# Performance work log

Hardware: AMD Instinct MI355X
Metric: run time of the kernel (lower is better)

The kernel has to match this reference:

```python
import jax, jax.numpy as jnp
import numpy as np

# module hyperparameters (init_kwargs)
WEIGHT = 2e-9
SIGMA_RGB = 0.15   # images in [0,1]; equals canonical 15/255
SIGMA_XY = 100.0
SCALE = 0.5

N, C, K, H, W = 4, 3, 21, 128, 128


def _nearest(x, oh, ow):
    """torch F.interpolate(mode='nearest'): src = floor(dst * in/out)."""
    h, w = x.shape[-2], x.shape[-1]
    iy = jnp.floor(jnp.arange(oh) * (h / oh)).astype(jnp.int32)
    ix = jnp.floor(jnp.arange(ow) * (w / ow)).astype(jnp.int32)
    return x[..., iy[:, None], ix[None, :]]


def _bilinear(x, oh, ow):
    """torch F.interpolate(mode='bilinear', align_corners=False)."""
    h, w = x.shape[-2], x.shape[-1]

    def coords(o, s):
        c = (jnp.arange(o, dtype=jnp.float32) + 0.5) * (s / o) - 0.5
        c = jnp.clip(c, 0.0, s - 1.0)
        c0 = jnp.floor(c).astype(jnp.int32)
        c1 = jnp.minimum(c0 + 1, s - 1)
        return c0, c1, c - c0

    y0, y1, wy = coords(oh, h)
    x0, x1, wx = coords(ow, w)
    wy = wy[:, None]
    wx = wx[None, :]
    v00 = x[..., y0[:, None], x0[None, :]]
    v01 = x[..., y0[:, None], x1[None, :]]
    v10 = x[..., y1[:, None], x0[None, :]]
    v11 = x[..., y1[:, None], x1[None, :]]
    top = v00 * (1.0 - wx) + v01 * wx
    bot = v10 * (1.0 - wx) + v11 * wx
    return top * (1.0 - wy) + bot * wy


def setup_inputs() -> dict:
    key = jax.random.key(0)
    k1, k2 = jax.random.split(key)
    images = jax.random.uniform(k1, (N, C, H, W), jnp.float32)
    segmentations = jax.random.uniform(k2, (N, K, H, W), jnp.float32)
    ROIs = jnp.ones((N, H, W), jnp.float32)
    return {"images": images, "segmentations": segmentations, "ROIs": ROIs}


def reference(images, segmentations, ROIs):
    oh, ow = int(H * SCALE), int(W * SCALE)
    img_s = _nearest(images, oh, ow)           # [N,3,oh,ow]
    seg_s = _bilinear(segmentations, oh, ow)   # [N,K,oh,ow]
    roi_s = _nearest(ROIs, oh, ow)             # [N,oh,ow]
    seg_m = seg_s * roi_s[:, None]             # seg * ROI (per class)
    sxy = SIGMA_XY * SCALE

    # exact dense Gaussian bilateral kernel that the permutohedral lattice
    # (bilateralfilter_batch) approximates: k(i,j) = exp(-|p_i-p_j|^2/(2 sxy^2)
    #                                                  -|I_i-I_j|^2/(2 srgb^2))
    yy, xx = jnp.meshgrid(jnp.arange(oh, dtype=jnp.float32),
                          jnp.arange(ow, dtype=jnp.float32), indexing="ij")
    pos = jnp.stack([xx, yy], 0) / sxy         # [2,oh,ow]

    def per_image(img, seg):
        feat = jnp.concatenate([pos, img / SIGMA_RGB], 0).reshape(5, -1).T  # [P,5]
        sq = jnp.sum(feat * feat, axis=-1)                                  # [P]
        d2 = jnp.maximum(sq[:, None] + sq[None, :] - 2.0 * (feat @ feat.T), 0.0)
        Wk = jnp.exp(-0.5 * d2)                                             # [P,P]
        s = seg.reshape(K, -1)                                              # [K,P]
        AS = s @ Wk                                                         # filtered seg
        return jnp.sum(s * AS)

    vals = jax.vmap(per_image)(img_s, seg_m)   # [N]
    loss = -(jnp.sum(vals)) / N                # densecrf_loss
    return WEIGHT * loss
```

## Files before the change

### kernel.cpp

```cpp
#include <hip/hip_runtime.h>

#define NIMG 4
#define CCH  3
#define KCH  21
#define HIN  128
#define WIN  128
#define OH   64
#define OW   64
#define PPX  (OH*OW)
#define NPIX (NIMG*PPX)

#define PRE2 1.20112241f

#define SEGW  24
#define FEATW 8

#define BLOCK  256
#define JCHUNK 256
#define IBLK   64

#define NSLOT  64

typedef _Float16 half_t;
typedef half_t half8  __attribute__((ext_vector_type(8)));
typedef float  f32x4v __attribute__((ext_vector_type(4)));

#define FEATH_OFF ((size_t)NPIX*SEGW*2)
#define SQF_OFF   (FEATH_OFF + (size_t)NPIX*FEATW*2)
#define SLOT_OFF  (SQF_OFF + (size_t)NPIX*4)

__global__ __launch_bounds__(BLOCK) void crf_prep(const float* __restrict__ img,
                                                  const float* __restrict__ seg,
                                                  const float* __restrict__ roi,
                                                  half_t* __restrict__ segH,
                                                  half_t* __restrict__ featH,
                                                  float* __restrict__ sqF,
                                                  float* __restrict__ slots) {
    int g  = blockIdx.x * BLOCK + threadIdx.x;
    int q  = g >> 14;
    int pl = g & (NPIX - 1);
    int n  = pl >> 12;
    int p  = pl & (PPX - 1);
    int y = p >> 6, x = p & 63;
    int y2 = 2 * y, x2 = 2 * x;

    if (q < SEGW) {
        float v = 0.0f;
        if (q < KCH) {
            const float* s0 = seg + (((size_t)n * KCH + q) * HIN + y2) * WIN + x2;
            float r = roi[((size_t)n * HIN + y2) * WIN + x2];
            v = 0.25f * (s0[0] + s0[1] + s0[WIN] + s0[WIN + 1]) * r;
        }
        segH[(size_t)pl * SEGW + q] = (half_t)v;
    } else if (q == 24) {
        float fx = (float)x * (PRE2 / 50.0f);
        float fy = (float)y * (PRE2 / 50.0f);
        const size_t ib = (((size_t)n * CCH) * HIN + y2) * WIN + x2;
        float fr = img[ib]                         * (PRE2 / 0.15f);
        float fg = img[ib + (size_t)HIN * WIN]     * (PRE2 / 0.15f);
        float fb = img[ib + 2 * (size_t)HIN * WIN] * (PRE2 / 0.15f);
        half_t h0 = (half_t)fx, h1 = (half_t)fy, h2 = (half_t)fr,
               h3 = (half_t)fg, h4 = (half_t)fb;
        half8 fh = {h0, h1, h2, h3, h4, (half_t)0, (half_t)0, (half_t)0};
        *(half8*)(featH + (size_t)pl * FEATW) = fh;
        float a0 = (float)h0, a1 = (float)h1, a2 = (float)h2,
              a3 = (float)h3, a4 = (float)h4;
        sqF[pl] = 0.5f * (a0 * a0 + a1 * a1 + a2 * a2 + a3 * a3 + a4 * a4);
    } else if (q == 25) {
        if (pl < NSLOT) slots[pl * 16] = 0.0f;
    }
}

__global__ __launch_bounds__(BLOCK, 8) void crf_main(const half_t* __restrict__ segH,
                                                     const half_t* __restrict__ featH,
                                                     const float* __restrict__ sqF,
                                                     float* __restrict__ slots) {
    const int bx = blockIdx.x;
    const int n  = blockIdx.y;

    int g = 0;
#pragma unroll
    for (int t = 1; t < 16; ++t) {
        int off = 64 * t - 2 * t * (t - 1);
        if (bx >= off) g = t;
    }
    int rem = bx - (64 * g - 2 * g * (g - 1));
    int c   = 16 - g;
    int iq  = (rem >= c) + (rem >= 2 * c) + (rem >= 3 * c);
    int I   = 4 * g + iq;
    int J   = g + (rem - iq * c);
    const bool diag = (J == (I >> 2));

    const half_t* segN  = segH  + (size_t)n * PPX * SEGW;
    const half_t* featN = featH + (size_t)n * PPX * FEATW;
    const float*  sqN   = sqF   + (size_t)n * PPX;

    __shared__ alignas(16) half_t segJ[JCHUNK * SEGW];
    __shared__ alignas(16) half_t featJ[JCHUNK * FEATW];
    __shared__ alignas(16) half_t zrow[8];
    __shared__ float hJ[JCHUNK];
    __shared__ float wsum[BLOCK / 64];

    const int tid  = threadIdx.x;
    const int lane = tid & 63, wv = tid >> 6;
    const int m = lane & 15, quad = lane >> 4;
    const int i0 = I * IBLK + wv * 16;
    const int j0 = J * JCHUNK;
    const int kq = (quad < 2) ? quad : 2;

    half8 hz = {};

    half8 aseg  = *(const half8*)(segN  + (size_t)(i0 + m) * SEGW + kq * 8);
    half8 afeat = *(const half8*)(featN + (size_t)(i0 + m) * FEATW);
    f32x4v hi   = *(const f32x4v*)(sqN + i0 + quad * 4);
    if (quad == 3) aseg  = hz;
    if (quad != 0) afeat = hz;
    f32x4v nh = -hi;

    {
        const f32x4v* gsrc = (const f32x4v*)(segN + (size_t)j0 * SEGW);
        f32x4v* ldst = (f32x4v*)segJ;
#pragma unroll
        for (int v = 0; v < 3; ++v) ldst[tid + v * BLOCK] = gsrc[tid + v * BLOCK];
        ((f32x4v*)featJ)[tid] = ((const f32x4v*)(featN + (size_t)j0 * FEATW))[tid];
        hJ[tid] = sqN[j0 + tid];
        if (tid < 8) zrow[tid] = (half_t)0;
    }
    __syncthreads();

    const half_t* bsp; int bstep;
    if (quad == 3) { bsp = zrow;                       bstep = 0; }
    else           { bsp = segJ + m * SEGW + quad * 8; bstep = 16 * SEGW; }
    const half_t* bfp; int fstep;
    if (quad == 0) { bfp = featJ + m * FEATW;          fstep = 16 * FEATW; }
    else           { bfp = zrow;                       fstep = 0; }

    float racc = 0.0f;
    const f32x4v zero4 = {0.0f, 0.0f, 0.0f, 0.0f};

#pragma unroll 4
    for (int jt = 0; jt < JCHUNK / 16; ++jt) {
        half8 bseg = *(const half8*)bsp;  bsp += bstep;
        half8 bft  = *(const half8*)bfp;  bfp += fstep;
        float hc = hJ[jt * 16 + m];

        f32x4v c4 = {nh[0] - hc, nh[1] - hc, nh[2] - hc, nh[3] - hc};
        f32x4v E  = __builtin_amdgcn_mfma_f32_16x16x32_f16(afeat, bft, c4, 0, 0, 0);
        f32x4v Gs = __builtin_amdgcn_mfma_f32_16x16x32_f16(aseg, bseg, zero4, 0, 0, 0);

        if (!diag) {
#pragma unroll
            for (int r = 0; r < 4; ++r)
                racc = fmaf(__builtin_amdgcn_exp2f(E[r]), Gs[r], racc);
        } else {
            const int jg = j0 + jt * 16 + m;
#pragma unroll
            for (int r = 0; r < 4; ++r) {
                int ig = i0 + quad * 4 + r;
                float sel = (jg > ig) ? 1.0f : ((jg == ig) ? 0.0f : -100000.0f);
                racc = fmaf(__builtin_amdgcn_exp2f(E[r] + sel), Gs[r], racc);
            }
        }
    }

#pragma unroll
    for (int off = 32; off > 0; off >>= 1) racc += __shfl_down(racc, off);
    if (lane == 0) wsum[wv] = racc;
    __syncthreads();
    if (tid == 0) {
        float s = wsum[0] + wsum[1] + wsum[2] + wsum[3];
        if (!diag) s *= 2.0f;
        int slot = (bx + 544 * n) & (NSLOT - 1);
        atomicAdd(&slots[slot * 16], s);
    }
}

__global__ __launch_bounds__(64) void crf_final(const float* __restrict__ slots,
                                                float* __restrict__ out) {
    int lane = threadIdx.x;
    float v = slots[lane * 16];
#pragma unroll
    for (int off = 32; off > 0; off >>= 1) v += __shfl_down(v, off);
    if (lane == 0) out[0] = v * (-5.0e-10f);
}

extern "C" void kernel_launch(void* const* d_in, const int* in_sizes, int n_in,
                              void* d_out, int out_size, void* d_ws, size_t ws_size,
                              hipStream_t stream) {
    const float* img = (const float*)d_in[0];
    const float* seg = (const float*)d_in[1];
    const float* roi = (const float*)d_in[2];
    float* out = (float*)d_out;

    char* wsb = (char*)d_ws;
    half_t* segH  = (half_t*)(wsb);
    half_t* featH = (half_t*)(wsb + FEATH_OFF);
    float*  sqF   = (float*)(wsb + SQF_OFF);
    float*  slots = (float*)(wsb + SLOT_OFF);

    crf_prep<<<(NPIX * 32) / BLOCK, BLOCK, 0, stream>>>(img, seg, roi,
                                                        segH, featH, sqF, slots);

    dim3 grid(544, NIMG);
    crf_main<<<grid, BLOCK, 0, stream>>>(segH, featH, sqF, slots);

    crf_final<<<1, 64, 0, stream>>>(slots, out);
}
```

Baseline: 76.42 us.

## Double i-rows per wave to reuse staged j-chunk across two MFMA tiles

Each wave now handles two 16-row i-tiles (IBLK 128) against the same shared j-chunk, so the j-side LDS staging and B-operand loads are reused twice and the grid shrinks to 272 blocks per image. The triangular block mapping is rewritten for the new tile shape. The single reduction chain is split into four independent accumulators to expose more ILP. Costs: more registers per thread (occupancy hint lowered to 6), fewer blocks to fill the GPU, and a coarser diagonal tile that does more masked work.

```diff
diff --git a/kernel.cpp b/kernel.cpp
--- a/kernel.cpp
+++ b/kernel.cpp
@@ -17,7 +17,7 @@
 
 #define BLOCK  256
 #define JCHUNK 256
-#define IBLK   64
+#define IBLK   128
 
 #define NSLOT  64
 
@@ -71,7 +71,7 @@
     }
 }
 
-__global__ __launch_bounds__(BLOCK, 8) void crf_main(const half_t* __restrict__ segH,
+__global__ __launch_bounds__(BLOCK, 6) void crf_main(const half_t* __restrict__ segH,
                                                      const half_t* __restrict__ featH,
                                                      const float* __restrict__ sqF,
                                                      float* __restrict__ slots) {
@@ -81,15 +81,15 @@
     int g = 0;
 #pragma unroll
     for (int t = 1; t < 16; ++t) {
-        int off = 64 * t - 2 * t * (t - 1);
+        int off = 32 * t - t * (t - 1);
         if (bx >= off) g = t;
     }
-    int rem = bx - (64 * g - 2 * g * (g - 1));
+    int rem = bx - (32 * g - g * (g - 1));
     int c   = 16 - g;
-    int iq  = (rem >= c) + (rem >= 2 * c) + (rem >= 3 * c);
-    int I   = 4 * g + iq;
+    int iq  = (rem >= c) ? 1 : 0;
+    int I   = 2 * g + iq;
     int J   = g + (rem - iq * c);
-    const bool diag = (J == (I >> 2));
+    const bool diag = (J == g);
 
     const half_t* segN  = segH  + (size_t)n * PPX * SEGW;
     const half_t* featN = featH + (size_t)n * PPX * FEATW;
@@ -110,12 +110,15 @@
 
     half8 hz = {};
 
-    half8 aseg  = *(const half8*)(segN  + (size_t)(i0 + m) * SEGW + kq * 8);
-    half8 afeat = *(const half8*)(featN + (size_t)(i0 + m) * FEATW);
-    f32x4v hi   = *(const f32x4v*)(sqN + i0 + quad * 4);
-    if (quad == 3) aseg  = hz;
-    if (quad != 0) afeat = hz;
-    f32x4v nh = -hi;
+    half8 aseg0  = *(const half8*)(segN  + (size_t)(i0 + m) * SEGW + kq * 8);
+    half8 aseg1  = *(const half8*)(segN  + (size_t)(i0 + 64 + m) * SEGW + kq * 8);
+    half8 afeat0 = *(const half8*)(featN + (size_t)(i0 + m) * FEATW);
+    half8 afeat1 = *(const half8*)(featN + (size_t)(i0 + 64 + m) * FEATW);
+    f32x4v hi0   = *(const f32x4v*)(sqN + i0 + quad * 4);
+    f32x4v hi1   = *(const f32x4v*)(sqN + i0 + 64 + quad * 4);
+    if (quad == 3) { aseg0 = hz; aseg1 = hz; }
+    if (quad != 0) { afeat0 = hz; afeat1 = hz; }
+    f32x4v nh0 = -hi0, nh1 = -hi1;
 
     {
         const f32x4v* gsrc = (const f32x4v*)(segN + (size_t)j0 * SEGW);
@@ -135,7 +138,7 @@
     if (quad == 0) { bfp = featJ + m * FEATW;          fstep = 16 * FEATW; }
     else           { bfp = zrow;                       fstep = 0; }
 
-    float racc = 0.0f;
+    float acc0 = 0.0f, acc1 = 0.0f, acc2 = 0.0f, acc3 = 0.0f;
     const f32x4v zero4 = {0.0f, 0.0f, 0.0f, 0.0f};
 
 #pragma unroll 4
@@ -144,25 +147,42 @@
         half8 bft  = *(const half8*)bfp;  bfp += fstep;
         float hc = hJ[jt * 16 + m];
 
-        f32x4v c4 = {nh[0] - hc, nh[1] - hc, nh[2] - hc, nh[3] - hc};
-        f32x4v E  = __builtin_amdgcn_mfma_f32_16x16x32_f16(afeat, bft, c4, 0, 0, 0);
-        f32x4v Gs = __builtin_amdgcn_mfma_f32_16x16x32_f16(aseg, bseg, zero4, 0, 0, 0);
+        f32x4v c40 = {nh0[0] - hc, nh0[1] - hc, nh0[2] - hc, nh0[3] - hc};
+        f32x4v c41 = {nh1[0] - hc, nh1[1] - hc, nh1[2] - hc, nh1[3] - hc};
+        f32x4v E0  = __builtin_amdgcn_mfma_f32_16x16x32_f16(afeat0, bft, c40, 0, 0, 0);
+        f32x4v E1  = __builtin_amdgcn_mfma_f32_16x16x32_f16(afeat1, bft, c41, 0, 0, 0);
+        f32x4v Gs0 = __builtin_amdgcn_mfma_f32_16x16x32_f16(aseg0, bseg, zero4, 0, 0, 0);
+        f32x4v Gs1 = __builtin_amdgcn_mfma_f32_16x16x32_f16(aseg1, bseg, zero4, 0, 0, 0);
 
         if (!diag) {
-#pragma unroll
-            for (int r = 0; r < 4; ++r)
-                racc = fmaf(__builtin_amdgcn_exp2f(E[r]), Gs[r], racc);
+            acc0 = fmaf(__builtin_amdgcn_exp2f(E0[0]), Gs0[0], acc0);
+            acc1 = fmaf(__builtin_amdgcn_exp2f(E0[1]), Gs0[1], acc1);
+            acc2 = fmaf(__builtin_amdgcn_exp2f(E0[2]), Gs0[2], acc2);
+            acc3 = fmaf(__builtin_amdgcn_exp2f(E0[3]), Gs0[3], acc3);
+            acc0 = fmaf(__builtin_amdgcn_exp2f(E1[0]), Gs1[0], acc0);
+            acc1 = fmaf(__builtin_amdgcn_exp2f(E1[1]), Gs1[1], acc1);
+            acc2 = fmaf(__builtin_amdgcn_exp2f(E1[2]), Gs1[2], acc2);
+            acc3 = fmaf(__builtin_amdgcn_exp2f(E1[3]), Gs1[3], acc3);
         } else {
             const int jg = j0 + jt * 16 + m;
+            const int ia = i0 + quad * 4;
 #pragma unroll
             for (int r = 0; r < 4; ++r) {
-                int ig = i0 + quad * 4 + r;
-                float sel = (jg > ig) ? 1.0f : ((jg == ig) ? 0.0f : -100000.0f);
-                racc = fmaf(__builtin_amdgcn_exp2f(E[r] + sel), Gs[r], racc);
+                int ig = ia + r;
+                float s0 = (jg > ig) ? 1.0f : ((jg == ig) ? 0.0f : -100000.0f);
+                int ig1 = ig + 64;
+                float s1 = (jg > ig1) ? 1.0f : ((jg == ig1) ? 0.0f : -100000.0f);
+                float t0 = fmaf(__builtin_amdgcn_exp2f(E0[r] + s0), Gs0[r], 0.0f);
+                float t1 = fmaf(__builtin_amdgcn_exp2f(E1[r] + s1), Gs1[r], 0.0f);
+                if (r == 0) acc0 += t0 + t1;
+                else if (r == 1) acc1 += t0 + t1;
+                else if (r == 2) acc2 += t0 + t1;
+                else acc3 += t0 + t1;
             }
         }
     }
 
+    float racc = (acc0 + acc1) + (acc2 + acc3);
 #pragma unroll
     for (int off = 32; off > 0; off >>= 1) racc += __shfl_down(racc, off);
     if (lane == 0) wsum[wv] = racc;
@@ -170,7 +190,7 @@
     if (tid == 0) {
         float s = wsum[0] + wsum[1] + wsum[2] + wsum[3];
         if (!diag) s *= 2.0f;
-        int slot = (bx + 544 * n) & (NSLOT - 1);
+        int slot = (bx + 272 * n) & (NSLOT - 1);
         atomicAdd(&slots[slot * 16], s);
     }
 }
@@ -201,7 +221,7 @@
     crf_prep<<<(NPIX * 32) / BLOCK, BLOCK, 0, stream>>>(img, seg, roi,
                                                         segH, featH, sqF, slots);
 
-    dim3 grid(544, NIMG);
+    dim3 grid(272, NIMG);
     crf_main<<<grid, BLOCK, 0, stream>>>(segH, featH, sqF, slots);
 
     crf_final<<<1, 64, 0, stream>>>(slots, out);
```

Result: no change. 76.51 us (+0.1%).

## Read MFMA B operands directly from global memory with zero-padded 32-wide records

Applied to the files above, without the earlier changes.

Pads the seg and feature records to 32 halves in the prep kernel (zero-filled) so every lane quad loads its MFMA operand straight from global/L2 memory with no per-quad masking. This removes the shared-memory staging of the J chunk and the block-wide barrier. It also splits the accumulator into four independent chains and lowers the launch-bounds occupancy hint from 8 to 4. The trade is more global traffic and a larger workspace, since padding grows the seg records from 24 to 32 and the feature records from 8 to 32, in exchange for no LDS or sync.

```diff
diff --git a/kernel.cpp b/kernel.cpp
--- a/kernel.cpp
+++ b/kernel.cpp
@@ -12,8 +12,7 @@
 
 #define PRE2 1.20112241f
 
-#define SEGW  24
-#define FEATW 8
+#define RECW  32
 
 #define BLOCK  256
 #define JCHUNK 256
@@ -25,8 +24,8 @@
 typedef half_t half8  __attribute__((ext_vector_type(8)));
 typedef float  f32x4v __attribute__((ext_vector_type(4)));
 
-#define FEATH_OFF ((size_t)NPIX*SEGW*2)
-#define SQF_OFF   (FEATH_OFF + (size_t)NPIX*FEATW*2)
+#define FEATH_OFF ((size_t)NPIX*RECW*2)
+#define SQF_OFF   (FEATH_OFF + (size_t)NPIX*RECW*2)
 #define SLOT_OFF  (SQF_OFF + (size_t)NPIX*4)
 
 __global__ __launch_bounds__(BLOCK) void crf_prep(const float* __restrict__ img,
@@ -44,15 +43,15 @@
     int y = p >> 6, x = p & 63;
     int y2 = 2 * y, x2 = 2 * x;
 
-    if (q < SEGW) {
+    if (q < RECW) {
         float v = 0.0f;
         if (q < KCH) {
             const float* s0 = seg + (((size_t)n * KCH + q) * HIN + y2) * WIN + x2;
             float r = roi[((size_t)n * HIN + y2) * WIN + x2];
             v = 0.25f * (s0[0] + s0[1] + s0[WIN] + s0[WIN + 1]) * r;
         }
-        segH[(size_t)pl * SEGW + q] = (half_t)v;
-    } else if (q == 24) {
+        segH[(size_t)pl * RECW + q] = (half_t)v;
+    } else if (q == 32) {
         float fx = (float)x * (PRE2 / 50.0f);
         float fy = (float)y * (PRE2 / 50.0f);
         const size_t ib = (((size_t)n * CCH) * HIN + y2) * WIN + x2;
@@ -62,16 +61,18 @@
         half_t h0 = (half_t)fx, h1 = (half_t)fy, h2 = (half_t)fr,
                h3 = (half_t)fg, h4 = (half_t)fb;
         half8 fh = {h0, h1, h2, h3, h4, (half_t)0, (half_t)0, (half_t)0};
-        *(half8*)(featH + (size_t)pl * FEATW) = fh;
+        *(half8*)(featH + (size_t)pl * RECW) = fh;
         float a0 = (float)h0, a1 = (float)h1, a2 = (float)h2,
               a3 = (float)h3, a4 = (float)h4;
         sqF[pl] = 0.5f * (a0 * a0 + a1 * a1 + a2 * a2 + a3 * a3 + a4 * a4);
-    } else if (q == 25) {
-        if (pl < NSLOT) slots[pl * 16] = 0.0f;
+    } else {
+        half8 z = {};
+        *(half8*)(featH + (size_t)pl * RECW + (q - 32) * 8) = z;
+        if (q == 35 && pl < NSLOT) slots[pl * 16] = 0.0f;
     }
 }
 
-__global__ __launch_bounds__(BLOCK, 8) void crf_main(const half_t* __restrict__ segH,
+__global__ __launch_bounds__(BLOCK, 4) void crf_main(const half_t* __restrict__ segH,
                                                      const half_t* __restrict__ featH,
                                                      const float* __restrict__ sqF,
                                                      float* __restrict__ slots) {
@@ -91,14 +92,10 @@
     int J   = g + (rem - iq * c);
     const bool diag = (J == (I >> 2));
 
-    const half_t* segN  = segH  + (size_t)n * PPX * SEGW;
-    const half_t* featN = featH + (size_t)n * PPX * FEATW;
+    const half_t* segN  = segH  + (size_t)n * PPX * RECW;
+    const half_t* featN = featH + (size_t)n * PPX * RECW;
     const float*  sqN   = sqF   + (size_t)n * PPX;
 
-    __shared__ alignas(16) half_t segJ[JCHUNK * SEGW];
-    __shared__ alignas(16) half_t featJ[JCHUNK * FEATW];
-    __shared__ alignas(16) half_t zrow[8];
-    __shared__ float hJ[JCHUNK];
     __shared__ float wsum[BLOCK / 64];
 
     const int tid  = threadIdx.x;
@@ -106,63 +103,49 @@
     const int m = lane & 15, quad = lane >> 4;
     const int i0 = I * IBLK + wv * 16;
     const int j0 = J * JCHUNK;
-    const int kq = (quad < 2) ? quad : 2;
 
-    half8 hz = {};
-
-    half8 aseg  = *(const half8*)(segN  + (size_t)(i0 + m) * SEGW + kq * 8);
-    half8 afeat = *(const half8*)(featN + (size_t)(i0 + m) * FEATW);
+    half8 aseg  = *(const half8*)(segN  + (size_t)(i0 + m) * RECW + quad * 8);
+    half8 afeat = *(const half8*)(featN + (size_t)(i0 + m) * RECW + quad * 8);
     f32x4v hi   = *(const f32x4v*)(sqN + i0 + quad * 4);
-    if (quad == 3) aseg  = hz;
-    if (quad != 0) afeat = hz;
     f32x4v nh = -hi;
 
-    {
-        const f32x4v* gsrc = (const f32x4v*)(segN + (size_t)j0 * SEGW);
-        f32x4v* ldst = (f32x4v*)segJ;
-#pragma unroll
-        for (int v = 0; v < 3; ++v) ldst[tid + v * BLOCK] = gsrc[tid + v * BLOCK];
-        ((f32x4v*)featJ)[tid] = ((const f32x4v*)(featN + (size_t)j0 * FEATW))[tid];
-        hJ[tid] = sqN[j0 + tid];
-        if (tid < 8) zrow[tid] = (half_t)0;
-    }
-    __syncthreads();
+    const half_t* bsp = segN  + (size_t)(j0 + m) * RECW + quad * 8;
+    const half_t* bfp = featN + (size_t)(j0 + m) * RECW + quad * 8;
+    const float*  hp  = sqN + j0 + m;
 
-    const half_t* bsp; int bstep;
-    if (quad == 3) { bsp = zrow;                       bstep = 0; }
-    else           { bsp = segJ + m * SEGW + quad * 8; bstep = 16 * SEGW; }
-    const half_t* bfp; int fstep;
-    if (quad == 0) { bfp = featJ + m * FEATW;          fstep = 16 * FEATW; }
-    else           { bfp = zrow;                       fstep = 0; }
-
-    float racc = 0.0f;
+    float acc0 = 0.0f, acc1 = 0.0f, acc2 = 0.0f, acc3 = 0.0f;
     const f32x4v zero4 = {0.0f, 0.0f, 0.0f, 0.0f};
 
 #pragma unroll 4
     for (int jt = 0; jt < JCHUNK / 16; ++jt) {
-        half8 bseg = *(const half8*)bsp;  bsp += bstep;
-        half8 bft  = *(const half8*)bfp;  bfp += fstep;
-        float hc = hJ[jt * 16 + m];
+        half8 bseg = *(const half8*)(bsp + (size_t)jt * 16 * RECW);
+        half8 bft  = *(const half8*)(bfp + (size_t)jt * 16 * RECW);
+        float hc   = hp[jt * 16];
 
         f32x4v c4 = {nh[0] - hc, nh[1] - hc, nh[2] - hc, nh[3] - hc};
         f32x4v E  = __builtin_amdgcn_mfma_f32_16x16x32_f16(afeat, bft, c4, 0, 0, 0);
         f32x4v Gs = __builtin_amdgcn_mfma_f32_16x16x32_f16(aseg, bseg, zero4, 0, 0, 0);
 
         if (!diag) {
-#pragma unroll
-            for (int r = 0; r < 4; ++r)
-                racc = fmaf(__builtin_amdgcn_exp2f(E[r]), Gs[r], racc);
+            acc0 = fmaf(__builtin_amdgcn_exp2f(E[0]), Gs[0], acc0);
+            acc1 = fmaf(__builtin_amdgcn_exp2f(E[1]), Gs[1], acc1);
+            acc2 = fmaf(__builtin_amdgcn_exp2f(E[2]), Gs[2], acc2);
+            acc3 = fmaf(__builtin_amdgcn_exp2f(E[3]), Gs[3], acc3);
         } else {
             const int jg = j0 + jt * 16 + m;
-#pragma unroll
-            for (int r = 0; r < 4; ++r) {
-                int ig = i0 + quad * 4 + r;
-                float sel = (jg > ig) ? 1.0f : ((jg == ig) ? 0.0f : -100000.0f);
-                racc = fmaf(__builtin_amdgcn_exp2f(E[r] + sel), Gs[r], racc);
-            }
+            const int ia = i0 + quad * 4;
+            float s0 = (jg > ia)     ? 1.0f : ((jg == ia)     ? 0.0f : -100000.0f);
+            float s1 = (jg > ia + 1) ? 1.0f : ((jg == ia + 1) ? 0.0f : -100000.0f);
+            float s2 = (jg > ia + 2) ? 1.0f : ((jg == ia + 2) ? 0.0f : -100000.0f);
+            float s3 = (jg > ia + 3) ? 1.0f : ((jg == ia + 3) ? 0.0f : -100000.0f);
+            acc0 = fmaf(__builtin_amdgcn_exp2f(E[0] + s0), Gs[0], acc0);
+            acc1 = fmaf(__builtin_amdgcn_exp2f(E[1] + s1), Gs[1], acc1);
+            acc2 = fmaf(__builtin_amdgcn_exp2f(E[2] + s2), Gs[2], acc2);
+            acc3 = fmaf(__builtin_amdgcn_exp2f(E[3] + s3), Gs[3], acc3);
         }
     }
 
+    float racc = (acc0 + acc1) + (acc2 + acc3);
 #pragma unroll
     for (int off = 32; off > 0; off >>= 1) racc += __shfl_down(racc, off);
     if (lane == 0) wsum[wv] = racc;
@@ -198,7 +181,7 @@
     float*  sqF   = (float*)(wsb + SQF_OFF);
     float*  slots = (float*)(wsb + SLOT_OFF);
 
-    crf_prep<<<(NPIX * 32) / BLOCK, BLOCK, 0, stream>>>(img, seg, roi,
+    crf_prep<<<(NPIX * 36) / BLOCK, BLOCK, 0, stream>>>(img, seg, roi,
                                                         segH, featH, sqF, slots);
 
     dim3 grid(544, NIMG);
```

Result: slower. 90.24 us (+18.1%).

## Enlarge CRF tiles to 256x256 with 1024-thread blocks and split accumulators

Applied to the files above, without the earlier changes.

The pairwise kernel now uses 1024-thread blocks, each covering a 256-row by 256-column tile. The triangular block enumeration is rewritten for 16x16 square tiles, which cuts the block count from 544 to 136 per image. The j-chunk staging into shared memory is amortised over four times as many rows, and the single serial FMA accumulator is split into four independent chains to expose instruction-level parallelism. In exchange there are far fewer, larger blocks, which risks a poor tail: blocks do not divide evenly over CUs, and diagonal blocks are uneven in cost. Register pressure also rises under the 1024-thread launch bound.

```diff
diff --git a/kernel.cpp b/kernel.cpp
--- a/kernel.cpp
+++ b/kernel.cpp
@@ -15,9 +15,9 @@
 #define SEGW  24
 #define FEATW 8
 
-#define BLOCK  256
+#define BLOCK  1024
 #define JCHUNK 256
-#define IBLK   64
+#define IBLK   256
 
 #define NSLOT  64
 
@@ -29,14 +29,14 @@
 #define SQF_OFF   (FEATH_OFF + (size_t)NPIX*FEATW*2)
 #define SLOT_OFF  (SQF_OFF + (size_t)NPIX*4)
 
-__global__ __launch_bounds__(BLOCK) void crf_prep(const float* __restrict__ img,
-                                                  const float* __restrict__ seg,
-                                                  const float* __restrict__ roi,
-                                                  half_t* __restrict__ segH,
-                                                  half_t* __restrict__ featH,
-                                                  float* __restrict__ sqF,
-                                                  float* __restrict__ slots) {
-    int g  = blockIdx.x * BLOCK + threadIdx.x;
+__global__ __launch_bounds__(256) void crf_prep(const float* __restrict__ img,
+                                                const float* __restrict__ seg,
+                                                const float* __restrict__ roi,
+                                                half_t* __restrict__ segH,
+                                                half_t* __restrict__ featH,
+                                                float* __restrict__ sqF,
+                                                float* __restrict__ slots) {
+    int g  = blockIdx.x * 256 + threadIdx.x;
     int q  = g >> 14;
     int pl = g & (NPIX - 1);
     int n  = pl >> 12;
@@ -78,18 +78,14 @@
     const int bx = blockIdx.x;
     const int n  = blockIdx.y;
 
-    int g = 0;
+    int I = 0;
 #pragma unroll
     for (int t = 1; t < 16; ++t) {
-        int off = 64 * t - 2 * t * (t - 1);
-        if (bx >= off) g = t;
-    }
-    int rem = bx - (64 * g - 2 * g * (g - 1));
-    int c   = 16 - g;
-    int iq  = (rem >= c) + (rem >= 2 * c) + (rem >= 3 * c);
-    int I   = 4 * g + iq;
-    int J   = g + (rem - iq * c);
-    const bool diag = (J == (I >> 2));
+        int off = 16 * t - (t * (t - 1)) / 2;
+        if (bx >= off) I = t;
+    }
+    int J = I + (bx - (16 * I - (I * (I - 1)) / 2));
+    const bool diag = (J == I);
 
     const half_t* segN  = segH  + (size_t)n * PPX * SEGW;
     const half_t* featN = featH + (size_t)n * PPX * FEATW;
@@ -118,12 +114,18 @@
     f32x4v nh = -hi;
 
     {
-        const f32x4v* gsrc = (const f32x4v*)(segN + (size_t)j0 * SEGW);
-        f32x4v* ldst = (f32x4v*)segJ;
-#pragma unroll
-        for (int v = 0; v < 3; ++v) ldst[tid + v * BLOCK] = gsrc[tid + v * BLOCK];
-        ((f32x4v*)featJ)[tid] = ((const f32x4v*)(featN + (size_t)j0 * FEATW))[tid];
-        hJ[tid] = sqN[j0 + tid];
+        if (tid < 768)
+            ((f32x4v*)segJ)[tid] = ((const f32x4v*)(segN + (size_t)j0 * SEGW))[tid];
+        else if (tid < 1024 - 8) {
+            int t = tid - 768;
+            if (t < 256)
+                ((f32x4v*)featJ)[t] = ((const f32x4v*)(featN + (size_t)j0 * FEATW))[t];
+        }
+        if (tid >= 1016) {
+            int t = tid - 1016 + 248;
+            ((f32x4v*)featJ)[t] = ((const f32x4v*)(featN + (size_t)j0 * FEATW))[t];
+        }
+        if (tid < 256) hJ[tid] = sqN[j0 + tid];
         if (tid < 8) zrow[tid] = (half_t)0;
     }
     __syncthreads();
@@ -135,7 +137,7 @@
     if (quad == 0) { bfp = featJ + m * FEATW;          fstep = 16 * FEATW; }
     else           { bfp = zrow;                       fstep = 0; }
 
-    float racc = 0.0f;
+    float acc0 = 0.0f, acc1 = 0.0f, acc2 = 0.0f, acc3 = 0.0f;
     const f32x4v zero4 = {0.0f, 0.0f, 0.0f, 0.0f};
 
 #pragma unroll 4
@@ -149,28 +151,35 @@
         f32x4v Gs = __builtin_amdgcn_mfma_f32_16x16x32_f16(aseg, bseg, zero4, 0, 0, 0);
 
         if (!diag) {
-#pragma unroll
-            for (int r = 0; r < 4; ++r)
-                racc = fmaf(__builtin_amdgcn_exp2f(E[r]), Gs[r], racc);
+            acc0 = fmaf(__builtin_amdgcn_exp2f(E[0]), Gs[0], acc0);
+            acc1 = fmaf(__builtin_amdgcn_exp2f(E[1]), Gs[1], acc1);
+            acc2 = fmaf(__builtin_amdgcn_exp2f(E[2]), Gs[2], acc2);
+            acc3 = fmaf(__builtin_amdgcn_exp2f(E[3]), Gs[3], acc3);
         } else {
             const int jg = j0 + jt * 16 + m;
-#pragma unroll
-            for (int r = 0; r < 4; ++r) {
-                int ig = i0 + quad * 4 + r;
-                float sel = (jg > ig) ? 1.0f : ((jg == ig) ? 0.0f : -100000.0f);
-                racc = fmaf(__builtin_amdgcn_exp2f(E[r] + sel), Gs[r], racc);
-            }
-        }
-    }
-
+            const int ia = i0 + quad * 4;
+            float s0 = (jg > ia)     ? 1.0f : ((jg == ia)     ? 0.0f : -100000.0f);
+            float s1 = (jg > ia + 1) ? 1.0f : ((jg == ia + 1) ? 0.0f : -100000.0f);
+            float s2 = (jg > ia + 2) ? 1.0f : ((jg == ia + 2) ? 0.0f : -100000.0f);
+            float s3 = (jg > ia + 3) ? 1.0f : ((jg == ia + 3) ? 0.0f : -100000.0f);
+            acc0 = fmaf(__builtin_amdgcn_exp2f(E[0] + s0), Gs[0], acc0);
+            acc1 = fmaf(__builtin_amdgcn_exp2f(E[1] + s1), Gs[1], acc1);
+            acc2 = fmaf(__builtin_amdgcn_exp2f(E[2] + s2), Gs[2], acc2);
+            acc3 = fmaf(__builtin_amdgcn_exp2f(E[3] + s3), Gs[3], acc3);
+        }
+    }
+
+    float racc = (acc0 + acc1) + (acc2 + acc3);
 #pragma unroll
     for (int off = 32; off > 0; off >>= 1) racc += __shfl_down(racc, off);
     if (lane == 0) wsum[wv] = racc;
     __syncthreads();
     if (tid == 0) {
-        float s = wsum[0] + wsum[1] + wsum[2] + wsum[3];
+        float s = 0.0f;
+#pragma unroll
+        for (int w = 0; w < BLOCK / 64; ++w) s += wsum[w];
         if (!diag) s *= 2.0f;
-        int slot = (bx + 544 * n) & (NSLOT - 1);
+        int slot = (bx + 136 * n) & (NSLOT - 1);
         atomicAdd(&slots[slot * 16], s);
     }
 }
@@ -198,10 +207,10 @@
     float*  sqF   = (float*)(wsb + SQF_OFF);
     float*  slots = (float*)(wsb + SLOT_OFF);
 
-    crf_prep<<<(NPIX * 32) / BLOCK, BLOCK, 0, stream>>>(img, seg, roi,
-                                                        segH, featH, sqF, slots);
-
-    dim3 grid(544, NIMG);
+    crf_prep<<<(NPIX * 32) / 256, 256, 0, stream>>>(img, seg, roi,
+                                                    segH, featH, sqF, slots);
+
+    dim3 grid(136, NIMG);
     crf_main<<<grid, BLOCK, 0, stream>>>(segH, featH, sqF, slots);
 
     crf_final<<<1, 64, 0, stream>>>(slots, out);
```

Result: slower. 79.85 us (+4.5%).
